# Performance work log

Measured on AMD Instinct MI355X. Metric: run time of the kernel, lower is better.

## Reference

```python
import jax, jax.numpy as jnp
import numpy as np

B, T, HID = 2, 2048, 2048
NH, NKV, D = 16, 4, 128
WIN = 512
ROPE_BASE = 10000.0
SCALE = D ** -0.5
EPS = 1e-12


def setup_inputs() -> dict:
    key = jax.random.key(0)
    ks = jax.random.split(key, 5)
    x = jax.random.normal(ks[0], (B, T, HID), dtype=jnp.float32)
    wq = jax.random.normal(ks[1], (HID, NH * D), dtype=jnp.float32) * 0.02
    wk = jax.random.normal(ks[2], (HID, NKV * D), dtype=jnp.float32) * 0.02
    wv = jax.random.normal(ks[3], (HID, NKV * D), dtype=jnp.float32) * 0.02
    wo = jax.random.normal(ks[4], (NH * D, HID), dtype=jnp.float32) * 0.02
    return {"x": x, "wq": wq, "wk": wk, "wv": wv, "wo": wo}


def _rope_tables(t, offset=0):
    inv_freq = 1.0 / (ROPE_BASE ** (jnp.arange(0, D, 2, dtype=jnp.float32) / D))
    pos = jnp.arange(offset, offset + t, dtype=jnp.float32)
    freqs = pos[:, None] * inv_freq[None, :]              # [t, D/2]
    cos = jnp.concatenate([jnp.cos(freqs), jnp.cos(freqs)], axis=-1)  # [t, D]
    sin = jnp.concatenate([jnp.sin(freqs), jnp.sin(freqs)], axis=-1)
    return cos, sin


def _apply_rope(x, cos, sin):
    # x: [B, H, T, D]; rotate-half formulation
    x1, x2 = jnp.split(x, 2, axis=-1)
    rot = jnp.concatenate([-x2, x1], axis=-1)
    return x * cos[None, None] + rot * sin[None, None]


def _l2norm(x):
    n = jnp.sqrt(jnp.sum(x * x, axis=-1, keepdims=True))
    return x / jnp.maximum(n, EPS)


def _forward(x, wq, wk, wv, wo):
    b, t, _ = x.shape
    q = (x @ wq).reshape(b, t, NH, D).transpose(0, 2, 1, 3)    # [B,H,T,D]
    k = (x @ wk).reshape(b, t, NKV, D).transpose(0, 2, 1, 3)   # [B,Hk,T,D]
    v = (x @ wv).reshape(b, t, NKV, D).transpose(0, 2, 1, 3)
    q = _l2norm(q)
    k = _l2norm(k)
    cos, sin = _rope_tables(t, offset=0)
    q = _apply_rope(q, cos, sin)
    k = _apply_rope(k, cos, sin)
    rep = NH // NKV
    k = jnp.repeat(k, rep, axis=1)                             # GQA repeat_interleave
    v = jnp.repeat(v, rep, axis=1)
    i = jnp.arange(t)
    allowed = (i[None, :] <= i[:, None]) & (i[None, :] > i[:, None] - WIN)  # [T,T]
    logits = jnp.einsum("bhid,bhjd->bhij", q, k) * SCALE
    logits = jnp.where(allowed[None, None], logits, -jnp.inf)
    attn = jax.nn.softmax(logits, axis=-1)
    out = jnp.einsum("bhij,bhjd->bhid", attn, v)
    out = out.transpose(0, 2, 1, 3).reshape(b, t, NH * D)
    return out @ wo


def reference(x, wq, wk, wv, wo):
    return _forward(x, wq, wk, wv, wo)
```

## Files before the change

kernel.cpp:

```cpp
#include <hip/hip_runtime.h>
#include <hip/hip_bf16.h>
#include <cstdint>

#define NHQ 16
#define NKVH 4
#define HDIM 128
#define WINSZ 512
#define TSEQ 2048
#define ATTN_SCALE 0.08838834764831845f

typedef __attribute__((ext_vector_type(8))) short s16x8;
typedef __attribute__((ext_vector_type(4))) float f32x4;

__device__ __forceinline__ void gload16(const void* g, void* lds) {
  __builtin_amdgcn_global_load_lds(
      (const __attribute__((address_space(1))) unsigned int*)g,
      (__attribute__((address_space(3))) unsigned int*)(uintptr_t)lds,
      16, 0, 0);
}

__device__ __forceinline__ f32x4 mfma16(s16x8 a, s16x8 b, f32x4 c) {
  return __builtin_amdgcn_mfma_f32_16x16x32_bf16(a, b, c, 0, 0, 0);
}

__global__ __launch_bounds__(256) void rope_tables_kernel(float* __restrict__ cosT,
                                                          float* __restrict__ sinT) {
  int idx = blockIdx.x * 256 + threadIdx.x;
  int t = idx >> 6, d2 = idx & 63;
  float inv = powf(10000.0f, -(float)d2 / 64.0f);
  float a = (float)t * inv;
  cosT[idx] = cosf(a);
  sinT[idx] = sinf(a);
}

__global__ __launch_bounds__(256) void cast_f32_bf16(const float* __restrict__ in,
                                                     __bf16* __restrict__ out, int n4) {
  int i = blockIdx.x * 256 + threadIdx.x;
  if (i >= n4) return;
  float4 v = ((const float4*)in)[i];
  __bf16 o[4];
  o[0] = (__bf16)v.x; o[1] = (__bf16)v.y; o[2] = (__bf16)v.z; o[3] = (__bf16)v.w;
  *(s16x8*)nullptr;
}

__global__ __launch_bounds__(256) void cast_kernel(const float* __restrict__ in,
                                                   __bf16* __restrict__ out, int n4) {
  int i = blockIdx.x * 256 + threadIdx.x;
  if (i >= n4) return;
  float4 v = ((const float4*)in)[i];
  union { __bf16 h[4]; uint2 u; } pk;
  pk.h[0] = (__bf16)v.x; pk.h[1] = (__bf16)v.y; pk.h[2] = (__bf16)v.z; pk.h[3] = (__bf16)v.w;
  ((uint2*)out)[i] = pk.u;
}

__global__ __launch_bounds__(256) void transpose_cast(const float* __restrict__ in,
                                                      __bf16* __restrict__ out, int R, int C) {
  __shared__ float tile[32][33];
  int c0 = blockIdx.x * 32, r0 = blockIdx.y * 32;
  int tx = threadIdx.x, ty = threadIdx.y;
#pragma unroll
  for (int i = 0; i < 4; i++)
    tile[ty + i * 8][tx] = in[(size_t)(r0 + ty + i * 8) * C + c0 + tx];
  __syncthreads();
#pragma unroll
  for (int i = 0; i < 4; i++)
    out[(size_t)(c0 + ty + i * 8) * R + r0 + tx] = (__bf16)tile[tx][ty + i * 8];
}

template <int MODE>
__global__ __launch_bounds__(256) void gemm_bt(const __bf16* __restrict__ A,
                                               const __bf16* __restrict__ Bt,
                                               float* __restrict__ Cf,
                                               __bf16* __restrict__ Qo, __bf16* __restrict__ Ko,
                                               __bf16* __restrict__ Vo, int M, int N, int K) {
  __shared__ __align__(16) __bf16 As[128 * 32];
  __shared__ __align__(16) __bf16 Bs[128 * 32];
  int tid = threadIdx.x;
  int w = tid >> 6, lane = tid & 63;
  int m0 = blockIdx.y * 128, n0 = blockIdx.x * 128;
  int wm = w >> 1, wn = w & 1;

  f32x4 acc[4][4];
  f32x4 zero = {0.f, 0.f, 0.f, 0.f};
#pragma unroll
  for (int i = 0; i < 4; i++)
#pragma unroll
    for (int j = 0; j < 4; j++) acc[i][j] = zero;

  int c0 = tid, c1 = tid + 256;
  const __bf16* ga0 = A + (size_t)(m0 + (c0 >> 2)) * K + (c0 & 3) * 8;
  const __bf16* ga1 = A + (size_t)(m0 + (c1 >> 2)) * K + (c1 & 3) * 8;
  const __bf16* gb0 = Bt + (size_t)(n0 + (c0 >> 2)) * K + (c0 & 3) * 8;
  const __bf16* gb1 = Bt + (size_t)(n0 + (c1 >> 2)) * K + (c1 & 3) * 8;
  char* lA = (char*)As + (size_t)w * 1024;
  char* lB = (char*)Bs + (size_t)w * 1024;

  for (int k0 = 0; k0 < K; k0 += 32) {
    __syncthreads();
    gload16(ga0 + k0, lA);
    gload16(ga1 + k0, lA + 4096);
    gload16(gb0 + k0, lB);
    gload16(gb1 + k0, lB + 4096);
    __syncthreads();
    s16x8 af[4], bfr[4];
#pragma unroll
    for (int mi = 0; mi < 4; mi++)
      af[mi] = *(const s16x8*)(As + (wm * 64 + mi * 16 + (lane & 15)) * 32 + (lane >> 4) * 8);
#pragma unroll
    for (int ni = 0; ni < 4; ni++)
      bfr[ni] = *(const s16x8*)(Bs + (wn * 64 + ni * 16 + (lane & 15)) * 32 + (lane >> 4) * 8);
#pragma unroll
    for (int mi = 0; mi < 4; mi++)
#pragma unroll
      for (int ni = 0; ni < 4; ni++)
        acc[mi][ni] = mfma16(af[mi], bfr[ni], acc[mi][ni]);
  }

#pragma unroll
  for (int mi = 0; mi < 4; mi++)
#pragma unroll
    for (int ni = 0; ni < 4; ni++) {
      int rbase = m0 + wm * 64 + mi * 16 + (lane >> 4) * 4;
      int col = n0 + wn * 64 + ni * 16 + (lane & 15);
#pragma unroll
      for (int r = 0; r < 4; r++) {
        int m = rbase + r;
        float v = acc[mi][ni][r];
        if constexpr (MODE == 0) {
          Cf[(size_t)m * N + col] = v;
        } else {
          int b = m >> 11, t = m & 2047;
          __bf16 bv = (__bf16)v;
          if (col < 2048) {
            Qo[(((size_t)(b * NHQ + (col >> 7))) * TSEQ + t) * HDIM + (col & 127)] = bv;
          } else if (col < 2560) {
            int c2 = col - 2048;
            Ko[(((size_t)(b * NKVH + (c2 >> 7))) * TSEQ + t) * HDIM + (c2 & 127)] = bv;
          } else {
            int c2 = col - 2560;
            Vo[(((size_t)(b * NKVH + (c2 >> 7))) * TSEQ + t) * HDIM + (c2 & 127)] = bv;
          }
        }
      }
    }
}

__global__ __launch_bounds__(256) void normrope(__bf16* __restrict__ Q, __bf16* __restrict__ Kk,
                                                const float* __restrict__ cosT,
                                                const float* __restrict__ sinT) {
  int w = threadIdx.x >> 6, lane = threadIdx.x & 63;
  int row = blockIdx.x / 5;
  int slot = (blockIdx.x % 5) * 4 + w;
  int b = row >> 11, t = row & 2047;
  __bf16* p;
  if (slot < 16)
    p = Q + (((size_t)(b * NHQ + slot)) * TSEQ + t) * HDIM;
  else
    p = Kk + (((size_t)(b * NKVH + (slot - 16))) * TSEQ + t) * HDIM;
  float x1 = (float)p[lane], x2 = (float)p[lane + 64];
  float ss = x1 * x1 + x2 * x2;
#pragma unroll
  for (int off = 32; off; off >>= 1) ss += __shfl_xor(ss, off);
  float inv = 1.0f / fmaxf(sqrtf(ss), 1e-12f);
  x1 *= inv;
  x2 *= inv;
  float c = cosT[t * 64 + lane], s = sinT[t * 64 + lane];
  p[lane] = (__bf16)(x1 * c - x2 * s);
  p[lane + 64] = (__bf16)(x2 * c + x1 * s);
}

__global__ __launch_bounds__(256) void attn_kernel(const __bf16* __restrict__ Qf,
                                                   const __bf16* __restrict__ Kf,
                                                   const __bf16* __restrict__ Vf,
                                                   __bf16* __restrict__ Ab) {
  __shared__ __align__(16) __bf16 Kl[32 * 136];
  __shared__ __align__(16) __bf16 Vt[128 * 40];
  __shared__ __align__(16) __bf16 Pl[4][16 * 40];
  int tid = threadIdx.x, w = tid >> 6, lane = tid & 63;
  int bid = blockIdx.x;
  int qt = bid & 31, h = (bid >> 5) & 15, b = bid >> 9;
  int qs = qt * 64;
  int kvh = h >> 2;
  const __bf16* Qb = Qf + ((size_t)(b * NHQ + h) * TSEQ) * HDIM;
  const __bf16* Kb = Kf + ((size_t)(b * NKVH + kvh) * TSEQ) * HDIM;
  const __bf16* Vb = Vf + ((size_t)(b * NKVH + kvh) * TSEQ) * HDIM;

  s16x8 aq[4];
  int qrow_f = qs + w * 16 + (lane & 15);
#pragma unroll
  for (int kb = 0; kb < 4; kb++)
    aq[kb] = *(const s16x8*)(Qb + (size_t)qrow_f * HDIM + kb * 32 + (lane >> 4) * 8);

  f32x4 acc[8];
  f32x4 zero = {0.f, 0.f, 0.f, 0.f};
#pragma unroll
  for (int db = 0; db < 8; db++) acc[db] = zero;
  float mrow[4], lrow[4];
#pragma unroll
  for (int r = 0; r < 4; r++) { mrow[r] = -1e30f; lrow[r] = 0.f; }

  int lo = qs - (WINSZ - 1);
  if (lo < 0) lo = 0;
  lo &= ~31;

  for (int ks = lo; ks <= qs + 63; ks += 32) {
    __syncthreads();
#pragma unroll
    for (int i = 0; i < 2; i++) {
      int c = tid + 256 * i;
      int j = c >> 4, dk = (c & 15) * 8;
      int4 kv = *(const int4*)(Kb + (size_t)(ks + j) * HDIM + dk);
      *(int4*)&Kl[j * 136 + dk] = kv;
      int jv = c & 31, d0 = (c >> 5) * 8;
      int4 vv = *(const int4*)(Vb + (size_t)(ks + jv) * HDIM + d0);
      const __bf16* pv = (const __bf16*)&vv;
#pragma unroll
      for (int e = 0; e < 8; e++) Vt[(d0 + e) * 40 + jv] = pv[e];
    }
    __syncthreads();

    f32x4 sacc[2];
    sacc[0] = zero; sacc[1] = zero;
#pragma unroll
    for (int jb = 0; jb < 2; jb++)
#pragma unroll
      for (int kb = 0; kb < 4; kb++) {
        s16x8 bk = *(const s16x8*)&Kl[(jb * 16 + (lane & 15)) * 136 + kb * 32 + (lane >> 4) * 8];
        sacc[jb] = mfma16(aq[kb], bk, sacc[jb]);
      }

    int colbase = ks + (lane & 15);
    float p0v[4], p1v[4], scf[4];
#pragma unroll
    for (int r = 0; r < 4; r++) {
      int qrow = qs + w * 16 + (lane >> 4) * 4 + r;
      float s0 = sacc[0][r] * ATTN_SCALE, s1 = sacc[1][r] * ATTN_SCALE;
      int j0 = colbase, j1 = colbase + 16;
      bool a0 = (j0 <= qrow) && (j0 > qrow - WINSZ);
      bool a1 = (j1 <= qrow) && (j1 > qrow - WINSZ);
      float mt = fmaxf(a0 ? s0 : -1e30f, a1 ? s1 : -1e30f);
#pragma unroll
      for (int off = 1; off < 16; off <<= 1) mt = fmaxf(mt, __shfl_xor(mt, off));
      float mn = fmaxf(mrow[r], mt);
      float p0 = a0 ? __expf(s0 - mn) : 0.f;
      float p1 = a1 ? __expf(s1 - mn) : 0.f;
      float sf = __expf(mrow[r] - mn);
      float ts = p0 + p1;
#pragma unroll
      for (int off = 1; off < 16; off <<= 1) ts += __shfl_xor(ts, off);
      lrow[r] = lrow[r] * sf + ts;
      mrow[r] = mn;
      p0v[r] = p0; p1v[r] = p1; scf[r] = sf;
    }

#pragma unroll
    for (int r = 0; r < 4; r++) {
      Pl[w][((lane >> 4) * 4 + r) * 40 + 0 * 16 + (lane & 15)] = (__bf16)p0v[r];
      Pl[w][((lane >> 4) * 4 + r) * 40 + 1 * 16 + (lane & 15)] = (__bf16)p1v[r];
    }
#pragma unroll
    for (int db = 0; db < 8; db++) {
      f32x4 t = acc[db];
#pragma unroll
      for (int r = 0; r < 4; r++) t[r] *= scf[r];
      acc[db] = t;
    }

    s16x8 pa = *(const s16x8*)&Pl[w][(lane & 15) * 40 + (lane >> 4) * 8];
#pragma unroll
    for (int db = 0; db < 8; db++) {
      s16x8 bv = *(const s16x8*)&Vt[(db * 16 + (lane & 15)) * 40 + (lane >> 4) * 8];
      acc[db] = mfma16(pa, bv, acc[db]);
    }
  }

#pragma unroll
  for (int db = 0; db < 8; db++)
#pragma unroll
    for (int r = 0; r < 4; r++) {
      int qrow = qs + w * 16 + (lane >> 4) * 4 + r;
      float v = acc[db][r] / lrow[r];
      Ab[((size_t)(b * TSEQ + qrow)) * 2048 + h * HDIM + db * 16 + (lane & 15)] = (__bf16)v;
    }
}

extern "C" void kernel_launch(void* const* d_in, const int* in_sizes, int n_in,
                              void* d_out, int out_size, void* d_ws, size_t ws_size,
                              hipStream_t stream) {
  const float* x = (const float*)d_in[0];
  const float* wq = (const float*)d_in[1];
  const float* wk = (const float*)d_in[2];
  const float* wv = (const float*)d_in[3];
  const float* wo = (const float*)d_in[4];
  float* out = (float*)d_out;

  char* ws = (char*)d_ws;
  size_t off = 0;
  auto alloc = [&](size_t bytes) -> void* {
    void* p = ws + off;
    off += (bytes + 255) & ~(size_t)255;
    return p;
  };
  __bf16* Xb = (__bf16*)alloc((size_t)4096 * 2048 * 2);
  __bf16* Wqkvt = (__bf16*)alloc((size_t)3072 * 2048 * 2);
  __bf16* Wot = (__bf16*)alloc((size_t)2048 * 2048 * 2);
  __bf16* Q = (__bf16*)alloc((size_t)2 * NHQ * TSEQ * HDIM * 2);
  __bf16* Kb = (__bf16*)alloc((size_t)2 * NKVH * TSEQ * HDIM * 2);
  __bf16* Vb = (__bf16*)alloc((size_t)2 * NKVH * TSEQ * HDIM * 2);
  float* cosT = (float*)alloc((size_t)TSEQ * 64 * 4);
  float* sinT = (float*)alloc((size_t)TSEQ * 64 * 4);
  __bf16* Ab = Xb;

  rope_tables_kernel<<<TSEQ * 64 / 256, 256, 0, stream>>>(cosT, sinT);
  cast_kernel<<<8192, 256, 0, stream>>>(x, Xb, 2097152);
  dim3 tb(32, 8);
  transpose_cast<<<dim3(64, 64), tb, 0, stream>>>(wq, Wqkvt, 2048, 2048);
  transpose_cast<<<dim3(16, 64), tb, 0, stream>>>(wk, Wqkvt + (size_t)2048 * 2048, 2048, 512);
  transpose_cast<<<dim3(16, 64), tb, 0, stream>>>(wv, Wqkvt + (size_t)2560 * 2048, 2048, 512);
  transpose_cast<<<dim3(64, 64), tb, 0, stream>>>(wo, Wot, 2048, 2048);

  gemm_bt<1><<<dim3(24, 32), 256, 0, stream>>>(Xb, Wqkvt, nullptr, Q, Kb, Vb, 4096, 3072, 2048);
  normrope<<<4096 * 5, 256, 0, stream>>>(Q, Kb, cosT, sinT);
  attn_kernel<<<2 * NHQ * (TSEQ / 64), 256, 0, stream>>>(Q, Kb, Vb, Ab);
  gemm_bt<0><<<dim3(16, 32), 256, 0, stream>>>(Ab, Wot, out, nullptr, nullptr, nullptr, 4096, 2048,
                                               2048);
}
```

Measured before the change: 239.3 us.

## Replace GEMM with 256x256-tile triple-buffered pipelined kernel with LDS swizzle

Replaces the 128x128 synchronous-load GEMM with a 512-thread 256x256 tile kernel. It triple-buffers LDS, issues global_load_lds prefetches two K-steps ahead under manual vmcnt waits and barriers, XOR-swizzles LDS to avoid bank conflicts, raises wave priority around MFMA blocks, and remaps block IDs across XCDs for L2 locality. The goal is to hide global-load latency and increase data reuse per tile in both projection GEMMs. The cost is more registers and LDS per block and far fewer blocks: 192 and 128, which is below the CU count for the output GEMM. It also removes a dead cast kernel.

```diff
diff --git a/kernel.cpp b/kernel.cpp
--- a/kernel.cpp
+++ b/kernel.cpp
@@ -22,6 +22,9 @@
 __device__ __forceinline__ f32x4 mfma16(s16x8 a, s16x8 b, f32x4 c) {
   return __builtin_amdgcn_mfma_f32_16x16x32_bf16(a, b, c, 0, 0, 0);
 }
+
+#define SBAR() asm volatile("s_barrier" ::: "memory")
+#define VMCNT(n) asm volatile("s_waitcnt vmcnt(" #n ")" ::: "memory")
 
 __global__ __launch_bounds__(256) void rope_tables_kernel(float* __restrict__ cosT,
                                                           float* __restrict__ sinT) {
@@ -33,16 +36,6 @@
   sinT[idx] = sinf(a);
 }
 
-__global__ __launch_bounds__(256) void cast_f32_bf16(const float* __restrict__ in,
-                                                     __bf16* __restrict__ out, int n4) {
-  int i = blockIdx.x * 256 + threadIdx.x;
-  if (i >= n4) return;
-  float4 v = ((const float4*)in)[i];
-  __bf16 o[4];
-  o[0] = (__bf16)v.x; o[1] = (__bf16)v.y; o[2] = (__bf16)v.z; o[3] = (__bf16)v.w;
-  *(s16x8*)nullptr;
-}
-
 __global__ __launch_bounds__(256) void cast_kernel(const float* __restrict__ in,
                                                    __bf16* __restrict__ out, int n4) {
   int i = blockIdx.x * 256 + threadIdx.x;
@@ -68,64 +61,111 @@
 }
 
 template <int MODE>
-__global__ __launch_bounds__(256) void gemm_bt(const __bf16* __restrict__ A,
-                                               const __bf16* __restrict__ Bt,
-                                               float* __restrict__ Cf,
-                                               __bf16* __restrict__ Qo, __bf16* __restrict__ Ko,
-                                               __bf16* __restrict__ Vo, int M, int N, int K) {
-  __shared__ __align__(16) __bf16 As[128 * 32];
-  __shared__ __align__(16) __bf16 Bs[128 * 32];
-  int tid = threadIdx.x;
-  int w = tid >> 6, lane = tid & 63;
-  int m0 = blockIdx.y * 128, n0 = blockIdx.x * 128;
-  int wm = w >> 1, wn = w & 1;
-
-  f32x4 acc[4][4];
+__global__ __launch_bounds__(512, 2) void gemm256(const __bf16* __restrict__ A,
+                                                  const __bf16* __restrict__ Bt,
+                                                  float* __restrict__ Cf,
+                                                  __bf16* __restrict__ Qo, __bf16* __restrict__ Ko,
+                                                  __bf16* __restrict__ Vo, int M, int N, int K) {
+  __shared__ __attribute__((aligned(16))) char Lds[3][2][16384];
+
+  const int tid = threadIdx.x;
+  const int w = tid >> 6, lane = tid & 63;
+  const int wm = w >> 2, wn = w & 3;
+
+  const int nbx = gridDim.x;
+  const int nwg = nbx * gridDim.y;
+  const int bid = blockIdx.y * nbx + blockIdx.x;
+  const int q8 = nwg >> 3, r8 = nwg & 7;
+  const int xcd = bid & 7, idx = bid >> 3;
+  const int swz = (xcd < r8 ? xcd * (q8 + 1) : r8 * (q8 + 1) + (xcd - r8) * q8) + idx;
+  const int bx = swz % nbx, by = swz / nbx;
+  const int m0 = by * 256, n0 = bx * 256;
+
+  const int r_st = tid >> 2;
+  const int c_src = (tid & 3) ^ ((tid >> 3) & 3);
+  const __bf16* gA = A + (size_t)(m0 + r_st) * K + c_src * 8;
+  const __bf16* gB = Bt + (size_t)(n0 + r_st) * K + c_src * 8;
+  const size_t hOF = (size_t)128 * K;
+
+  auto stA = [&](int t, int h, int b) {
+    gload16(gA + h * hOF + t * 32, Lds[b][0] + h * 8192 + w * 1024);
+  };
+  auto stB = [&](int t, int h, int b) {
+    gload16(gB + h * hOF + t * 32, Lds[b][1] + h * 8192 + w * 1024);
+  };
+
+  const int swzr = (((lane >> 4) ^ (((lane & 15) >> 1) & 3)) << 4);
+  const int aoff = wm * 8192 + (lane & 15) * 64 + swzr;
+  const int boff = (wn >> 1) * 8192 + (wn & 1) * 4096 + (lane & 15) * 64 + swzr;
+
+  f32x4 acc[8][4];
   f32x4 zero = {0.f, 0.f, 0.f, 0.f};
 #pragma unroll
-  for (int i = 0; i < 4; i++)
+  for (int i = 0; i < 8; i++)
 #pragma unroll
     for (int j = 0; j < 4; j++) acc[i][j] = zero;
 
-  int c0 = tid, c1 = tid + 256;
-  const __bf16* ga0 = A + (size_t)(m0 + (c0 >> 2)) * K + (c0 & 3) * 8;
-  const __bf16* ga1 = A + (size_t)(m0 + (c1 >> 2)) * K + (c1 & 3) * 8;
-  const __bf16* gb0 = Bt + (size_t)(n0 + (c0 >> 2)) * K + (c0 & 3) * 8;
-  const __bf16* gb1 = Bt + (size_t)(n0 + (c1 >> 2)) * K + (c1 & 3) * 8;
-  char* lA = (char*)As + (size_t)w * 1024;
-  char* lB = (char*)Bs + (size_t)w * 1024;
-
-  for (int k0 = 0; k0 < K; k0 += 32) {
-    __syncthreads();
-    gload16(ga0 + k0, lA);
-    gload16(ga1 + k0, lA + 4096);
-    gload16(gb0 + k0, lB);
-    gload16(gb1 + k0, lB + 4096);
-    __syncthreads();
-    s16x8 af[4], bfr[4];
-#pragma unroll
-    for (int mi = 0; mi < 4; mi++)
-      af[mi] = *(const s16x8*)(As + (wm * 64 + mi * 16 + (lane & 15)) * 32 + (lane >> 4) * 8);
-#pragma unroll
-    for (int ni = 0; ni < 4; ni++)
-      bfr[ni] = *(const s16x8*)(Bs + (wn * 64 + ni * 16 + (lane & 15)) * 32 + (lane >> 4) * 8);
-#pragma unroll
-    for (int mi = 0; mi < 4; mi++)
-#pragma unroll
-      for (int ni = 0; ni < 4; ni++)
-        acc[mi][ni] = mfma16(af[mi], bfr[ni], acc[mi][ni]);
+  const int NT = K >> 5;
+
+  stA(0, 0, 0); stA(0, 1, 0); stB(0, 0, 0); stB(0, 1, 0);
+  stA(1, 0, 1); stA(1, 1, 1); stB(1, 0, 1);
+  VMCNT(3);
+  SBAR();
+
+  int cur = 0;
+  for (int t = 0; t < NT; ++t) {
+    int nb1 = cur + 1; if (nb1 == 3) nb1 = 0;
+    int nb2 = nb1 + 1; if (nb2 == 3) nb2 = 0;
+    const char* bA = Lds[cur][0];
+    const char* bB = Lds[cur][1];
+
+    s16x8 fb[4], fa[4];
+#pragma unroll
+    for (int nf = 0; nf < 4; nf++) fb[nf] = *(const s16x8*)(bB + boff + nf * 1024);
+#pragma unroll
+    for (int mf = 0; mf < 4; mf++) fa[mf] = *(const s16x8*)(bA + aoff + mf * 1024);
+    if (t + 1 < NT) stB(t + 1, 1, nb1);
+    if (t + 2 < NT) stA(t + 2, 0, nb2);
+    SBAR();
+    __builtin_amdgcn_s_setprio(1);
+#pragma unroll
+    for (int mf = 0; mf < 4; mf++)
+#pragma unroll
+      for (int nf = 0; nf < 4; nf++) acc[mf][nf] = mfma16(fa[mf], fb[nf], acc[mf][nf]);
+    __builtin_amdgcn_s_setprio(0);
+    SBAR();
+
+#pragma unroll
+    for (int mf = 0; mf < 4; mf++) fa[mf] = *(const s16x8*)(bA + aoff + 4096 + mf * 1024);
+    if (t + 2 < NT) { stA(t + 2, 1, nb2); stB(t + 2, 0, nb2); }
+    SBAR();
+    __builtin_amdgcn_s_setprio(1);
+#pragma unroll
+    for (int mf = 0; mf < 4; mf++)
+#pragma unroll
+      for (int nf = 0; nf < 4; nf++) acc[4 + mf][nf] = mfma16(fa[mf], fb[nf], acc[4 + mf][nf]);
+    __builtin_amdgcn_s_setprio(0);
+
+    if (t < NT - 2) {
+      VMCNT(3);
+      SBAR();
+    } else if (t == NT - 2) {
+      VMCNT(0);
+      SBAR();
+    }
+    cur = nb1;
   }
 
 #pragma unroll
-  for (int mi = 0; mi < 4; mi++)
-#pragma unroll
-    for (int ni = 0; ni < 4; ni++) {
-      int rbase = m0 + wm * 64 + mi * 16 + (lane >> 4) * 4;
-      int col = n0 + wn * 64 + ni * 16 + (lane & 15);
+  for (int mf = 0; mf < 8; mf++)
+#pragma unroll
+    for (int nf = 0; nf < 4; nf++) {
+      int rbase = m0 + wm * 128 + mf * 16 + (lane >> 4) * 4;
+      int col = n0 + wn * 64 + nf * 16 + (lane & 15);
 #pragma unroll
       for (int r = 0; r < 4; r++) {
         int m = rbase + r;
-        float v = acc[mi][ni][r];
+        float v = acc[mf][nf][r];
         if constexpr (MODE == 0) {
           Cf[(size_t)m * N + col] = v;
         } else {
@@ -319,9 +359,9 @@
   transpose_cast<<<dim3(16, 64), tb, 0, stream>>>(wv, Wqkvt + (size_t)2560 * 2048, 2048, 512);
   transpose_cast<<<dim3(64, 64), tb, 0, stream>>>(wo, Wot, 2048, 2048);
 
-  gemm_bt<1><<<dim3(24, 32), 256, 0, stream>>>(Xb, Wqkvt, nullptr, Q, Kb, Vb, 4096, 3072, 2048);
+  gemm256<1><<<dim3(12, 16), 512, 0, stream>>>(Xb, Wqkvt, nullptr, Q, Kb, Vb, 4096, 3072, 2048);
   normrope<<<4096 * 5, 256, 0, stream>>>(Q, Kb, cosT, sinT);
   attn_kernel<<<2 * NHQ * (TSEQ / 64), 256, 0, stream>>>(Q, Kb, Vb, Ab);
-  gemm_bt<0><<<dim3(16, 32), 256, 0, stream>>>(Ab, Wot, out, nullptr, nullptr, nullptr, 4096, 2048,
-                                               2048);
-}
+  gemm256<0><<<dim3(8, 16), 512, 0, stream>>>(Ab, Wot, out, nullptr, nullptr, nullptr, 4096, 2048,
+                                              2048);
+}
```

Measured after the change: 240.4 us. About the same (+0.5%).
